# Kernel optimization log

Measured on AMD Instinct MI355X. Metric: run time of the kernel, lower is better.

## Reference

```python
import jax, jax.numpy as jnp
import numpy as np

B, CAP, H, NH = 128, 65536, 512, 8
HD = H // NH
GH = H // 4  # gate hidden


def setup_inputs() -> dict:
    key = jax.random.key(0)
    ks = jax.random.split(key, 8)
    s = 1.0 / np.sqrt(H)
    sg = 1.0 / np.sqrt(GH)
    return {
        "query": jax.random.normal(ks[0], (B, H), jnp.float32),
        "memory_keys": jax.random.normal(ks[1], (CAP, H), jnp.float32) * s,
        "memory_values": jax.random.normal(ks[2], (CAP, H), jnp.float32) * s,
        "in_proj_w": jax.random.normal(ks[3], (3 * H, H), jnp.float32) * s,
        "in_proj_b": jnp.zeros((3 * H,), jnp.float32),
        "out_proj_w": jax.random.normal(ks[4], (H, H), jnp.float32) * s,
        "out_proj_b": jnp.zeros((H,), jnp.float32),
        "gate_w1": jax.random.normal(ks[5], (GH, H), jnp.float32) * s,
        "gate_b1": jnp.zeros((GH,), jnp.float32),
        "gate_w2": jax.random.normal(ks[6], (1, GH), jnp.float32) * sg,
        "gate_b2": jnp.zeros((1,), jnp.float32),
        "usage_count": jnp.zeros((CAP,), jnp.float32),
        "last_used": jnp.zeros((CAP,), jnp.float32),
        "step_counter": 1,
    }


def reference(query, memory_keys, memory_values, in_proj_w, in_proj_b,
              out_proj_w, out_proj_b, gate_w1, gate_b1, gate_w2, gate_b2,
              usage_count, last_used, step_counter):
    # nn.MultiheadAttention packed projections: rows [0:H]=Wq, [H:2H]=Wk, [2H:3H]=Wv
    wq, wk, wv = in_proj_w[:H], in_proj_w[H:2 * H], in_proj_w[2 * H:]
    bq, bk, bv = in_proj_b[:H], in_proj_b[H:2 * H], in_proj_b[2 * H:]

    q = (query @ wq.T + bq).reshape(B, NH, HD)           # [B, h, d] (q_len = 1)
    k = (memory_keys @ wk.T + bk).reshape(CAP, NH, HD)   # [C, h, d]
    v = (memory_values @ wv.T + bv).reshape(CAP, NH, HD)  # [C, h, d]

    scores = jnp.einsum('bhd,chd->bhc', q, k) / np.sqrt(HD)  # [B, h, C]
    attn = jax.nn.softmax(scores, axis=-1)
    ctx = jnp.einsum('bhc,chd->bhd', attn, v).reshape(B, H)
    attn_out = ctx @ out_proj_w.T + out_proj_b               # [B, H]

    # usage bookkeeping: attn_weights averaged over heads, then over batch
    avg_attn = attn.mean(axis=(0, 1))                        # [C]
    new_usage = usage_count + avg_attn
    new_last = jnp.where(avg_attn > 1e-3,
                         jnp.float32(step_counter), last_used)

    # gating MLP: Linear -> ReLU -> Linear -> Sigmoid
    gate = jax.nn.sigmoid(
        jax.nn.relu(query @ gate_w1.T + gate_b1) @ gate_w2.T + gate_b2)  # [B, 1]
    memory_output = gate * attn_out                          # [B, H]
    return memory_output, new_usage, new_last
```

## Files before the change

kernel.cpp:

```cpp
#include <hip/hip_runtime.h>
#include <stdint.h>


typedef __bf16 b16x8 __attribute__((ext_vector_type(8)));
typedef float f32x4 __attribute__((ext_vector_type(4)));

static __device__ __forceinline__ unsigned short f2bf(float f) {
  return __builtin_bit_cast(unsigned short, (__bf16)f);
}

static __device__ __forceinline__ f32x4 MFMA(b16x8 a, b16x8 b, f32x4 c) {
  return __builtin_amdgcn_mfma_f32_16x16x32_bf16(a, b, c, 0, 0, 0);
}

#define GLL16(g, l)                                                          \
  __builtin_amdgcn_global_load_lds(                                          \
      (const __attribute__((address_space(1))) void*)(g),                    \
      (__attribute__((address_space(3))) void*)(l), 16, 0, 0)

#define SBAR() __builtin_amdgcn_sched_barrier(0)

__global__ void k_convert_w(const float* __restrict__ w, unsigned short* __restrict__ dst) {
  int i = blockIdx.x * 256 + threadIdx.x;
  float4 v = reinterpret_cast<const float4*>(w + 512 * 512)[i];
  ushort4 o;
  o.x = f2bf(v.x); o.y = f2bf(v.y); o.z = f2bf(v.z); o.w = f2bf(v.w);
  reinterpret_cast<ushort4*>(dst)[i] = o;
}

__global__ void k_proj_q(const float* __restrict__ query, const float* __restrict__ w,
                         const float* __restrict__ bias, unsigned short* __restrict__ qout) {
  __shared__ float qs[512];
  int b = blockIdx.x, j = threadIdx.x;
  qs[j] = query[b * 512 + j];
  __syncthreads();
  float acc = bias[j];
  const float4* q4 = reinterpret_cast<const float4*>(qs);
  const float4* w4 = reinterpret_cast<const float4*>(w + j * 512);
#pragma unroll 8
  for (int i = 0; i < 128; ++i) {
    float4 a = q4[i], c = w4[i];
    acc += a.x * c.x + a.y * c.y + a.z * c.z + a.w * c.w;
  }
  qout[b * 512 + j] = f2bf(acc);
}

__global__ void k_gate(const float* __restrict__ query, const float* __restrict__ w1,
                       const float* __restrict__ b1, const float* __restrict__ w2,
                       const float* __restrict__ b2, float* __restrict__ gate) {
  __shared__ float qs[512];
  __shared__ float red[2];
  int b = blockIdx.x, j = threadIdx.x;
  qs[j] = query[b * 512 + j];
  qs[j + 128] = query[b * 512 + j + 128];
  qs[j + 256] = query[b * 512 + j + 256];
  qs[j + 384] = query[b * 512 + j + 384];
  __syncthreads();
  float acc = b1[j];
  const float4* q4 = reinterpret_cast<const float4*>(qs);
  const float4* w4 = reinterpret_cast<const float4*>(w1 + j * 512);
#pragma unroll 8
  for (int i = 0; i < 128; ++i) {
    float4 a = q4[i], c = w4[i];
    acc += a.x * c.x + a.y * c.y + a.z * c.z + a.w * c.w;
  }
  float t = fmaxf(acc, 0.f) * w2[j];
#pragma unroll
  for (int off = 1; off < 64; off <<= 1) t += __shfl_xor(t, off, 64);
  if ((j & 63) == 0) red[j >> 6] = t;
  __syncthreads();
  if (j == 0) {
    float z = red[0] + red[1] + b2[0];
    gate[b] = 1.f / (1.f + __builtin_amdgcn_exp2f(-z * 1.44269504088896f));
  }
}

__global__ __launch_bounds__(512, 2) void k_proj_kv(
    const float* __restrict__ mk, const float* __restrict__ mv,
    const unsigned short* __restrict__ wkb, const unsigned short* __restrict__ wvb,
    const float* __restrict__ in_b,
    unsigned short* __restrict__ kout, unsigned short* __restrict__ vtout) {
  const int p = blockIdx.x;
  const int isV = p & 1;
  const int c0 = (p >> 1) * 128;
  const float* Ag = isV ? mv : mk;
  const unsigned short* W = isV ? wvb : wkb;
  const float* bias = in_b + (isV ? 1024 : 512);
  const int tid = threadIdx.x;
  const int w = tid >> 6, lane = tid & 63;
  const int wr = w >> 2, wc = w & 3;
  const int ln = tid & 15, g = (tid & 63) >> 4;

  __shared__ __align__(16) unsigned short AL[65536];
  __shared__ __align__(16) unsigned short WL[4][4096];

  const int wrow = 16 * w + (lane >> 2);
  const int wcs = (lane & 3) ^ ((wrow >> 1) & 3);
  const unsigned short* wsrc = W + (size_t)wrow * 512 + wcs * 8;
  const int wdst = w * 512;

  GLL16(wsrc, &WL[0][wdst]);
  GLL16(wsrc + 32, &WL[1][wdst]);

#pragma unroll 4
  for (int c = 0; c < 16; ++c) {
    int row = c * 8 + w;
    const float* src = Ag + (size_t)(c0 + row) * 512 + lane * 8;
    float4 f0 = *reinterpret_cast<const float4*>(src);
    float4 f1 = *reinterpret_cast<const float4*>(src + 4);
    b16x8 v;
    v[0] = (__bf16)f0.x; v[1] = (__bf16)f0.y; v[2] = (__bf16)f0.z; v[3] = (__bf16)f0.w;
    v[4] = (__bf16)f1.x; v[5] = (__bf16)f1.y; v[6] = (__bf16)f1.z; v[7] = (__bf16)f1.w;
    int chunk = lane ^ (row & 7);
    *reinterpret_cast<b16x8*>(&AL[row * 512 + chunk * 8]) = v;
  }
  __syncthreads();

#pragma unroll
  for (int jt = 0; jt < 4; ++jt) {
    const int j0 = jt * 128;
    f32x4 acc[4][2];
#pragma unroll
    for (int m = 0; m < 4; ++m)
#pragma unroll
      for (int n = 0; n < 2; ++n) acc[m][n] = {0.f, 0.f, 0.f, 0.f};

#pragma unroll
    for (int kk = 0; kk < 16; ++kk) {
      const int t = jt * 16 + kk;
      const int tn = (t + 2 <= 63) ? t + 2 : 63;
      const int slot = (t + 2) & 3;
      GLL16(wsrc + (size_t)(tn >> 4) * 65536 + (tn & 15) * 32, &WL[slot][wdst]);
      SBAR();
      asm volatile("s_waitcnt vmcnt(2)" ::: "memory");
      SBAR();
      __builtin_amdgcn_s_barrier();
      SBAR();
      b16x8 af[4], wf[2];
#pragma unroll
      for (int m = 0; m < 4; ++m) {
        int r = 64 * wr + 16 * m + ln;
        int ch = (kk * 4 + g) ^ (r & 7);
        af[m] = *reinterpret_cast<const b16x8*>(&AL[r * 512 + ch * 8]);
      }
#pragma unroll
      for (int n = 0; n < 2; ++n) {
        int r = 32 * wc + 16 * n + ln;
        wf[n] = *reinterpret_cast<const b16x8*>(&WL[t & 3][r * 32 + ((g ^ ((r >> 1) & 3)) << 3)]);
      }
      if (!isV) {
#pragma unroll
        for (int m = 0; m < 4; ++m)
#pragma unroll
          for (int n = 0; n < 2; ++n) acc[m][n] = MFMA(wf[n], af[m], acc[m][n]);
      } else {
#pragma unroll
        for (int m = 0; m < 4; ++m)
#pragma unroll
          for (int n = 0; n < 2; ++n) acc[m][n] = MFMA(af[m], wf[n], acc[m][n]);
      }
    }

    if (!isV) {
#pragma unroll
      for (int m = 0; m < 4; ++m) {
        int c = c0 + 64 * wr + 16 * m + ln;
#pragma unroll
        for (int n = 0; n < 2; ++n) {
          int jb = j0 + 32 * wc + 16 * n + 4 * g;
          float4 bb = *reinterpret_cast<const float4*>(&bias[jb]);
          ushort4 o;
          o.x = f2bf(acc[m][n][0] + bb.x);
          o.y = f2bf(acc[m][n][1] + bb.y);
          o.z = f2bf(acc[m][n][2] + bb.z);
          o.w = f2bf(acc[m][n][3] + bb.w);
          *reinterpret_cast<ushort4*>(&kout[(size_t)c * 512 + jb]) = o;
        }
      }
    } else {
#pragma unroll
      for (int n = 0; n < 2; ++n) {
        int j = j0 + 32 * wc + 16 * n + ln;
        float bj = bias[j];
#pragma unroll
        for (int m = 0; m < 4; ++m) {
          int cb = c0 + 64 * wr + 16 * m + 4 * g;
          ushort4 o;
          o.x = f2bf(acc[m][n][0] + bj);
          o.y = f2bf(acc[m][n][1] + bj);
          o.z = f2bf(acc[m][n][2] + bj);
          o.w = f2bf(acc[m][n][3] + bj);
          *reinterpret_cast<ushort4*>(&vtout[(size_t)j * 65536 + cb]) = o;
        }
      }
    }
  }
  asm volatile("s_waitcnt vmcnt(0)" ::: "memory");
}

__global__ __launch_bounds__(256) void k_attn1(
    const unsigned short* __restrict__ kb, const unsigned short* __restrict__ vt,
    const unsigned short* __restrict__ qb,
    float* __restrict__ l_ws, float* __restrict__ ctxT) {
  const int h = blockIdx.y, cg = blockIdx.x;
  const int tid = threadIdx.x;
  const int wv = tid >> 6, wr = wv >> 1, wc = wv & 1;
  const int ln = tid & 15, g = (tid & 63) >> 4;
  __shared__ __align__(16) unsigned short kS[128 * 64];
  __shared__ __align__(16) unsigned short pS[128 * 128];
  __shared__ __align__(16) unsigned short vS[64 * 128];
  const float SC = 0.125f * 1.44269504088896f;

  b16x8 qf[4][2];
#pragma unroll
  for (int n = 0; n < 4; ++n)
#pragma unroll
    for (int ks = 0; ks < 2; ++ks) {
      int b = 64 * wc + 16 * n + ln;
      qf[n][ks] = *reinterpret_cast<const b16x8*>(&qb[(size_t)b * 512 + h * 64 + ks * 32 + g * 8]);
    }
  f32x4 pacc[2][4];
#pragma unroll
  for (int m = 0; m < 2; ++m)
#pragma unroll
    for (int n = 0; n < 4; ++n) pacc[m][n] = {0.f, 0.f, 0.f, 0.f};
  float lsum[4] = {0.f, 0.f, 0.f, 0.f};

  for (int it = 0; it < 8; ++it) {
    int c0g = cg * 1024 + it * 128;
#pragma unroll
    for (int i = 0; i < 4; ++i) {
      int fl = i * 256 + tid, row = fl >> 3, p8 = fl & 7;
      uint4 d = *reinterpret_cast<const uint4*>(&kb[(size_t)(c0g + row) * 512 + h * 64 + p8 * 8]);
      *reinterpret_cast<uint4*>(&kS[(row * 8 + (p8 ^ (row & 7))) * 8]) = d;
    }
#pragma unroll
    for (int i = 0; i < 4; ++i) {
      int fl = i * 256 + tid, row = fl >> 4, p16 = fl & 15;
      uint4 d = *reinterpret_cast<const uint4*>(&vt[(size_t)(h * 64 + row) * 65536 + c0g + p16 * 8]);
      *reinterpret_cast<uint4*>(&vS[(row * 16 + (p16 ^ (row & 7))) * 8]) = d;
    }
    __syncthreads();

    f32x4 sacc[4][4];
#pragma unroll
    for (int m = 0; m < 4; ++m)
#pragma unroll
      for (int n = 0; n < 4; ++n) sacc[m][n] = {0.f, 0.f, 0.f, 0.f};
#pragma unroll
    for (int ks = 0; ks < 2; ++ks) {
      b16x8 a[4];
#pragma unroll
      for (int m = 0; m < 4; ++m) {
        int row = 64 * wr + 16 * m + ln;
        a[m] = *reinterpret_cast<const b16x8*>(&kS[(row * 8 + ((ks * 4 + g) ^ (row & 7))) * 8]);
      }
#pragma unroll
      for (int m = 0; m < 4; ++m)
#pragma unroll
        for (int n = 0; n < 4; ++n) sacc[m][n] = MFMA(a[m], qf[n][ks], sacc[m][n]);
    }
#pragma unroll
    for (int m = 0; m < 4; ++m)
#pragma unroll
      for (int n = 0; n < 4; ++n) {
        float p0 = __builtin_amdgcn_exp2f(sacc[m][n][0] * SC);
        float p1 = __builtin_amdgcn_exp2f(sacc[m][n][1] * SC);
        float p2 = __builtin_amdgcn_exp2f(sacc[m][n][2] * SC);
        float p3 = __builtin_amdgcn_exp2f(sacc[m][n][3] * SC);
        lsum[n] += (p0 + p1) + (p2 + p3);
        int b = 64 * wc + 16 * n + ln;
        int c = 64 * wr + 16 * m + 4 * g;
        int base = b * 128 + (((c >> 3) ^ (b & 7)) * 8) + (c & 7);
        ushort2 lo, hi;
        lo.x = f2bf(p0); lo.y = f2bf(p1);
        hi.x = f2bf(p2); hi.y = f2bf(p3);
        *reinterpret_cast<ushort2*>(&pS[base]) = lo;
        *reinterpret_cast<ushort2*>(&pS[base + 2]) = hi;
      }
    __syncthreads();
#pragma unroll
    for (int ks = 0; ks < 4; ++ks) {
      b16x8 av[2], bp[4];
#pragma unroll
      for (int m = 0; m < 2; ++m) {
        int row = 32 * wr + 16 * m + ln;
        av[m] = *reinterpret_cast<const b16x8*>(&vS[(row * 16 + ((ks * 4 + g) ^ (row & 7))) * 8]);
      }
#pragma unroll
      for (int n = 0; n < 4; ++n) {
        int row = 64 * wc + 16 * n + ln;
        bp[n] = *reinterpret_cast<const b16x8*>(&pS[(row * 16 + ((ks * 4 + g) ^ (row & 7))) * 8]);
      }
#pragma unroll
      for (int m = 0; m < 2; ++m)
#pragma unroll
        for (int n = 0; n < 4; ++n) pacc[m][n] = MFMA(av[m], bp[n], pacc[m][n]);
    }
    __syncthreads();
  }
#pragma unroll
  for (int n = 0; n < 4; ++n) {
    float v = lsum[n];
    v += __shfl_xor(v, 16, 64);
    v += __shfl_xor(v, 32, 64);
    if ((tid & 63) < 16) atomicAdd(&l_ws[h * 128 + 64 * wc + 16 * n + ln], v);
  }
#pragma unroll
  for (int m = 0; m < 2; ++m)
#pragma unroll
    for (int n = 0; n < 4; ++n)
#pragma unroll
      for (int r = 0; r < 4; ++r) {
        int d = 32 * wr + 16 * m + 4 * g + r;
        int b = 64 * wc + 16 * n + ln;
        atomicAdd(&ctxT[(h * 64 + d) * 128 + b], pacc[m][n][r]);
      }
}

__global__ __launch_bounds__(256) void k_attn2(
    const unsigned short* __restrict__ kb, const unsigned short* __restrict__ qb,
    const float* __restrict__ l_ws, float* __restrict__ avgA) {
  const int h = blockIdx.y, cg = blockIdx.x;
  const int tid = threadIdx.x;
  const int wv = tid >> 6, wr = wv >> 1, wc = wv & 1;
  const int ln = tid & 15, g = (tid & 63) >> 4;
  __shared__ __align__(16) unsigned short kS[128 * 64];
  __shared__ float wS[128];
  const float SC = 0.125f * 1.44269504088896f;
  if (tid < 128) wS[tid] = 1.f / l_ws[h * 128 + tid];
  b16x8 qf[4][2];
#pragma unroll
  for (int n = 0; n < 4; ++n)
#pragma unroll
    for (int ks = 0; ks < 2; ++ks) {
      int b = 64 * wc + 16 * n + ln;
      qf[n][ks] = *reinterpret_cast<const b16x8*>(&qb[(size_t)b * 512 + h * 64 + ks * 32 + g * 8]);
    }
  __syncthreads();
  float wn[4];
#pragma unroll
  for (int n = 0; n < 4; ++n) wn[n] = wS[64 * wc + 16 * n + ln];

  for (int it = 0; it < 8; ++it) {
    int c0g = cg * 1024 + it * 128;
#pragma unroll
    for (int i = 0; i < 4; ++i) {
      int fl = i * 256 + tid, row = fl >> 3, p8 = fl & 7;
      uint4 d = *reinterpret_cast<const uint4*>(&kb[(size_t)(c0g + row) * 512 + h * 64 + p8 * 8]);
      *reinterpret_cast<uint4*>(&kS[(row * 8 + (p8 ^ (row & 7))) * 8]) = d;
    }
    __syncthreads();
    f32x4 sacc[4][4];
#pragma unroll
    for (int m = 0; m < 4; ++m)
#pragma unroll
      for (int n = 0; n < 4; ++n) sacc[m][n] = {0.f, 0.f, 0.f, 0.f};
#pragma unroll
    for (int ks = 0; ks < 2; ++ks) {
      b16x8 a[4];
#pragma unroll
      for (int m = 0; m < 4; ++m) {
        int row = 64 * wr + 16 * m + ln;
        a[m] = *reinterpret_cast<const b16x8*>(&kS[(row * 8 + ((ks * 4 + g) ^ (row & 7))) * 8]);
      }
#pragma unroll
      for (int m = 0; m < 4; ++m)
#pragma unroll
        for (int n = 0; n < 4; ++n) sacc[m][n] = MFMA(a[m], qf[n][ks], sacc[m][n]);
    }
#pragma unroll
    for (int m = 0; m < 4; ++m) {
      float s0 = 0.f, s1 = 0.f, s2 = 0.f, s3 = 0.f;
#pragma unroll
      for (int n = 0; n < 4; ++n) {
        s0 += __builtin_amdgcn_exp2f(sacc[m][n][0] * SC) * wn[n];
        s1 += __builtin_amdgcn_exp2f(sacc[m][n][1] * SC) * wn[n];
        s2 += __builtin_amdgcn_exp2f(sacc[m][n][2] * SC) * wn[n];
        s3 += __builtin_amdgcn_exp2f(sacc[m][n][3] * SC) * wn[n];
      }
#pragma unroll
      for (int off = 1; off < 16; off <<= 1) {
        s0 += __shfl_xor(s0, off, 64);
        s1 += __shfl_xor(s1, off, 64);
        s2 += __shfl_xor(s2, off, 64);
        s3 += __shfl_xor(s3, off, 64);
      }
      if (ln == 0) {
        int c = c0g + 64 * wr + 16 * m + 4 * g;
        atomicAdd(&avgA[c], s0);
        atomicAdd(&avgA[c + 1], s1);
        atomicAdd(&avgA[c + 2], s2);
        atomicAdd(&avgA[c + 3], s3);
      }
    }
    __syncthreads();
  }
}

__global__ void k_finalize(const float* __restrict__ ctxT, const float* __restrict__ l_ws,
                           const float* __restrict__ wout, const float* __restrict__ bout,
                           const float* __restrict__ gate, float* __restrict__ out) {
  __shared__ float cs[512];
  int b = blockIdx.x, j = threadIdx.x;
  cs[j] = ctxT[j * 128 + b] / l_ws[(j >> 6) * 128 + b];
  __syncthreads();
  float acc = bout[j];
  const float4* c4 = reinterpret_cast<const float4*>(cs);
  const float4* w4 = reinterpret_cast<const float4*>(wout + j * 512);
#pragma unroll 8
  for (int i = 0; i < 128; ++i) {
    float4 a = c4[i], c = w4[i];
    acc += a.x * c.x + a.y * c.y + a.z * c.z + a.w * c.w;
  }
  out[b * 512 + j] = gate[b] * acc;
}

__global__ void k_usage(const float* __restrict__ avgA, const float* __restrict__ usage,
                        const float* __restrict__ last, const int* __restrict__ step,
                        float* __restrict__ out_usage, float* __restrict__ out_last) {
  int c = blockIdx.x * 256 + threadIdx.x;
  float avg = avgA[c] * (1.f / 1024.f);
  out_usage[c] = usage[c] + avg;
  out_last[c] = (avg > 0.001f) ? (float)step[0] : last[c];
}

extern "C" void kernel_launch(void* const* d_in, const int* in_sizes, int n_in,
                              void* d_out, int out_size, void* d_ws, size_t ws_size,
                              hipStream_t stream) {
  const float* query = (const float*)d_in[0];
  const float* mk    = (const float*)d_in[1];
  const float* mv    = (const float*)d_in[2];
  const float* in_w  = (const float*)d_in[3];
  const float* in_b  = (const float*)d_in[4];
  const float* out_w = (const float*)d_in[5];
  const float* out_b = (const float*)d_in[6];
  const float* gw1   = (const float*)d_in[7];
  const float* gb1   = (const float*)d_in[8];
  const float* gw2   = (const float*)d_in[9];
  const float* gb2   = (const float*)d_in[10];
  const float* usage = (const float*)d_in[11];
  const float* last  = (const float*)d_in[12];
  const int*   step  = (const int*)d_in[13];

  char* ws = (char*)d_ws;
  unsigned short* qb  = (unsigned short*)(ws);
  unsigned short* wkb = (unsigned short*)(ws + 131072);
  unsigned short* wvb = (unsigned short*)(ws + 655360);
  unsigned short* kb  = (unsigned short*)(ws + 1179648);
  unsigned short* vt  = (unsigned short*)(ws + 68288512);
  float* l_ws = (float*)(ws + 135397376);
  float* ctxT = (float*)(ws + 135401472);
  float* avgA = (float*)(ws + 135663616);
  float* gate = (float*)(ws + 135925760);
  float* out = (float*)d_out;

  hipMemsetAsync(ws + 135397376, 0, 4096 + 262144 + 262144, stream);

  k_convert_w<<<512, 256, 0, stream>>>(in_w, wkb);
  k_proj_q<<<128, 512, 0, stream>>>(query, in_w, in_b, qb);
  k_gate<<<128, 128, 0, stream>>>(query, gw1, gb1, gw2, gb2, gate);
  k_proj_kv<<<1024, 512, 0, stream>>>(mk, mv, wkb, wvb, in_b, kb, vt);
  k_attn1<<<dim3(64, 8), 256, 0, stream>>>(kb, vt, qb, l_ws, ctxT);
  k_attn2<<<dim3(64, 8), 256, 0, stream>>>(kb, qb, l_ws, avgA);
  k_finalize<<<128, 512, 0, stream>>>(ctxT, l_ws, out_w, out_b, gate, out);
  k_usage<<<256, 256, 0, stream>>>(avgA, usage, last, step, out + 65536, out + 131072);
}
```

Before: 345.7 us.

## Batch small GEMV kernels by 8 rows and give each wave private weight buffers

The q-projection, gate and finalize kernels now each handle 8 batch rows per block, so every weight row read from global memory is reused 8 times and the grid shrinks from 128 to 16 blocks. In the K/V projection kernel each wave now stages its own slice of the weight tile into a per-wave double buffer instead of a shared 4-slot ring, which removes the block-wide s_barrier on every k-step. The cost is fewer blocks (less parallelism) in the small kernels, and the per-wave buffers load weight rows redundantly across waves. The launch bound changes from 2 to 1 blocks per CU.

```diff
diff --git a/kernel.cpp b/kernel.cpp
--- a/kernel.cpp
+++ b/kernel.cpp
@@ -28,54 +28,77 @@
   reinterpret_cast<ushort4*>(dst)[i] = o;
 }
 
-__global__ void k_proj_q(const float* __restrict__ query, const float* __restrict__ w,
-                         const float* __restrict__ bias, unsigned short* __restrict__ qout) {
-  __shared__ float qs[512];
-  int b = blockIdx.x, j = threadIdx.x;
-  qs[j] = query[b * 512 + j];
+__global__ __launch_bounds__(512) void k_proj_q(const float* __restrict__ query,
+                                                const float* __restrict__ w,
+                                                const float* __restrict__ bias,
+                                                unsigned short* __restrict__ qout) {
+  __shared__ float qs[8][512];
+  const int b0 = blockIdx.x * 8, t = threadIdx.x;
+#pragma unroll
+  for (int r = 0; r < 8; ++r) qs[r][t] = query[(size_t)(b0 + r) * 512 + t];
   __syncthreads();
-  float acc = bias[j];
-  const float4* q4 = reinterpret_cast<const float4*>(qs);
-  const float4* w4 = reinterpret_cast<const float4*>(w + j * 512);
-#pragma unroll 8
+  const int j = t;
+  float bj = bias[j];
+  float acc[8];
+#pragma unroll
+  for (int r = 0; r < 8; ++r) acc[r] = bj;
+  const float4* w4 = reinterpret_cast<const float4*>(w + (size_t)j * 512);
+#pragma unroll 4
   for (int i = 0; i < 128; ++i) {
-    float4 a = q4[i], c = w4[i];
-    acc += a.x * c.x + a.y * c.y + a.z * c.z + a.w * c.w;
-  }
-  qout[b * 512 + j] = f2bf(acc);
+    float4 c = w4[i];
+#pragma unroll
+    for (int r = 0; r < 8; ++r) {
+      float4 a = reinterpret_cast<const float4*>(qs[r])[i];
+      acc[r] += a.x * c.x + a.y * c.y + a.z * c.z + a.w * c.w;
+    }
+  }
+#pragma unroll
+  for (int r = 0; r < 8; ++r) qout[(size_t)(b0 + r) * 512 + j] = f2bf(acc[r]);
 }
 
 __global__ void k_gate(const float* __restrict__ query, const float* __restrict__ w1,
                        const float* __restrict__ b1, const float* __restrict__ w2,
                        const float* __restrict__ b2, float* __restrict__ gate) {
-  __shared__ float qs[512];
-  __shared__ float red[2];
-  int b = blockIdx.x, j = threadIdx.x;
-  qs[j] = query[b * 512 + j];
-  qs[j + 128] = query[b * 512 + j + 128];
-  qs[j + 256] = query[b * 512 + j + 256];
-  qs[j + 384] = query[b * 512 + j + 384];
+  __shared__ float qs[8][512];
+  __shared__ float red[2][8];
+  const int b0 = blockIdx.x * 8, t = threadIdx.x;
+#pragma unroll
+  for (int u = 0; u < 32; ++u) {
+    int idx = u * 128 + t;
+    qs[idx >> 9][idx & 511] = query[(size_t)(b0 + (idx >> 9)) * 512 + (idx & 511)];
+  }
   __syncthreads();
-  float acc = b1[j];
-  const float4* q4 = reinterpret_cast<const float4*>(qs);
-  const float4* w4 = reinterpret_cast<const float4*>(w1 + j * 512);
-#pragma unroll 8
+  const int j = t;
+  float bj = b1[j];
+  float acc[8];
+#pragma unroll
+  for (int r = 0; r < 8; ++r) acc[r] = bj;
+  const float4* w4 = reinterpret_cast<const float4*>(w1 + (size_t)j * 512);
+#pragma unroll 4
   for (int i = 0; i < 128; ++i) {
-    float4 a = q4[i], c = w4[i];
-    acc += a.x * c.x + a.y * c.y + a.z * c.z + a.w * c.w;
-  }
-  float t = fmaxf(acc, 0.f) * w2[j];
-#pragma unroll
-  for (int off = 1; off < 64; off <<= 1) t += __shfl_xor(t, off, 64);
-  if ((j & 63) == 0) red[j >> 6] = t;
+    float4 c = w4[i];
+#pragma unroll
+    for (int r = 0; r < 8; ++r) {
+      float4 a = reinterpret_cast<const float4*>(qs[r])[i];
+      acc[r] += a.x * c.x + a.y * c.y + a.z * c.z + a.w * c.w;
+    }
+  }
+  float w2j = w2[j];
+#pragma unroll
+  for (int r = 0; r < 8; ++r) {
+    float v = fmaxf(acc[r], 0.f) * w2j;
+#pragma unroll
+    for (int off = 1; off < 64; off <<= 1) v += __shfl_xor(v, off, 64);
+    if ((t & 63) == 0) red[t >> 6][r] = v;
+  }
   __syncthreads();
-  if (j == 0) {
-    float z = red[0] + red[1] + b2[0];
-    gate[b] = 1.f / (1.f + __builtin_amdgcn_exp2f(-z * 1.44269504088896f));
-  }
-}
-
-__global__ __launch_bounds__(512, 2) void k_proj_kv(
+  if (t < 8) {
+    float z = red[0][t] + red[1][t] + b2[0];
+    gate[b0 + t] = 1.f / (1.f + __builtin_amdgcn_exp2f(-z * 1.44269504088896f));
+  }
+}
+
+__global__ __launch_bounds__(512, 1) void k_proj_kv(
     const float* __restrict__ mk, const float* __restrict__ mv,
     const unsigned short* __restrict__ wkb, const unsigned short* __restrict__ wvb,
     const float* __restrict__ in_b,
@@ -92,15 +115,14 @@
   const int ln = tid & 15, g = (tid & 63) >> 4;
 
   __shared__ __align__(16) unsigned short AL[65536];
-  __shared__ __align__(16) unsigned short WL[4][4096];
-
-  const int wrow = 16 * w + (lane >> 2);
-  const int wcs = (lane & 3) ^ ((wrow >> 1) & 3);
-  const unsigned short* wsrc = W + (size_t)wrow * 512 + wcs * 8;
-  const int wdst = w * 512;
-
-  GLL16(wsrc, &WL[0][wdst]);
-  GLL16(wsrc + 32, &WL[1][wdst]);
+  __shared__ __align__(16) unsigned short WLp[8][2][1024];
+
+  const int srw0 = 32 * wc + ln;
+  const int srw1 = srw0 + 16;
+  const int colo = g * 8;
+
+  GLL16(W + (size_t)srw0 * 512 + colo, &WLp[w][0][0]);
+  GLL16(W + (size_t)srw1 * 512 + colo, &WLp[w][0][512]);
 
 #pragma unroll 4
   for (int c = 0; c < 16; ++c) {
@@ -118,7 +140,6 @@
 
 #pragma unroll
   for (int jt = 0; jt < 4; ++jt) {
-    const int j0 = jt * 128;
     f32x4 acc[4][2];
 #pragma unroll
     for (int m = 0; m < 4; ++m)
@@ -128,13 +149,13 @@
 #pragma unroll
     for (int kk = 0; kk < 16; ++kk) {
       const int t = jt * 16 + kk;
-      const int tn = (t + 2 <= 63) ? t + 2 : 63;
-      const int slot = (t + 2) & 3;
-      GLL16(wsrc + (size_t)(tn >> 4) * 65536 + (tn & 15) * 32, &WL[slot][wdst]);
+      const int tn = (t < 63) ? t + 1 : 63;
+      const int sl = (t + 1) & 1;
+      const int jn = tn >> 4, kn = tn & 15;
+      GLL16(W + (size_t)(jn * 128 + srw0) * 512 + kn * 32 + colo, &WLp[w][sl][0]);
+      GLL16(W + (size_t)(jn * 128 + srw1) * 512 + kn * 32 + colo, &WLp[w][sl][512]);
       SBAR();
       asm volatile("s_waitcnt vmcnt(2)" ::: "memory");
-      SBAR();
-      __builtin_amdgcn_s_barrier();
       SBAR();
       b16x8 af[4], wf[2];
 #pragma unroll
@@ -144,10 +165,8 @@
         af[m] = *reinterpret_cast<const b16x8*>(&AL[r * 512 + ch * 8]);
       }
 #pragma unroll
-      for (int n = 0; n < 2; ++n) {
-        int r = 32 * wc + 16 * n + ln;
-        wf[n] = *reinterpret_cast<const b16x8*>(&WL[t & 3][r * 32 + ((g ^ ((r >> 1) & 3)) << 3)]);
-      }
+      for (int n = 0; n < 2; ++n)
+        wf[n] = *reinterpret_cast<const b16x8*>(&WLp[w][t & 1][n * 512 + lane * 8]);
       if (!isV) {
 #pragma unroll
         for (int m = 0; m < 4; ++m)
@@ -161,6 +180,7 @@
       }
     }
 
+    const int j0 = jt * 128;
     if (!isV) {
 #pragma unroll
       for (int m = 0; m < 4; ++m) {
@@ -398,22 +418,35 @@
   }
 }
 
-__global__ void k_finalize(const float* __restrict__ ctxT, const float* __restrict__ l_ws,
-                           const float* __restrict__ wout, const float* __restrict__ bout,
-                           const float* __restrict__ gate, float* __restrict__ out) {
-  __shared__ float cs[512];
-  int b = blockIdx.x, j = threadIdx.x;
-  cs[j] = ctxT[j * 128 + b] / l_ws[(j >> 6) * 128 + b];
+__global__ __launch_bounds__(512) void k_finalize(
+    const float* __restrict__ ctxT, const float* __restrict__ l_ws,
+    const float* __restrict__ wout, const float* __restrict__ bout,
+    const float* __restrict__ gate, float* __restrict__ out) {
+  __shared__ float cs[8][512];
+  const int b0 = blockIdx.x * 8, t = threadIdx.x;
+#pragma unroll
+  for (int r = 0; r < 8; ++r) {
+    int b = b0 + r;
+    cs[r][t] = ctxT[t * 128 + b] / l_ws[(t >> 6) * 128 + b];
+  }
   __syncthreads();
-  float acc = bout[j];
-  const float4* c4 = reinterpret_cast<const float4*>(cs);
-  const float4* w4 = reinterpret_cast<const float4*>(wout + j * 512);
-#pragma unroll 8
+  const int j = t;
+  float bj = bout[j];
+  float acc[8];
+#pragma unroll
+  for (int r = 0; r < 8; ++r) acc[r] = bj;
+  const float4* w4 = reinterpret_cast<const float4*>(wout + (size_t)j * 512);
+#pragma unroll 4
   for (int i = 0; i < 128; ++i) {
-    float4 a = c4[i], c = w4[i];
-    acc += a.x * c.x + a.y * c.y + a.z * c.z + a.w * c.w;
-  }
-  out[b * 512 + j] = gate[b] * acc;
+    float4 c = w4[i];
+#pragma unroll
+    for (int r = 0; r < 8; ++r) {
+      float4 a = reinterpret_cast<const float4*>(cs[r])[i];
+      acc[r] += a.x * c.x + a.y * c.y + a.z * c.z + a.w * c.w;
+    }
+  }
+#pragma unroll
+  for (int r = 0; r < 8; ++r) out[(size_t)(b0 + r) * 512 + j] = gate[b0 + r] * acc[r];
 }
 
 __global__ void k_usage(const float* __restrict__ avgA, const float* __restrict__ usage,
@@ -458,11 +491,11 @@
   hipMemsetAsync(ws + 135397376, 0, 4096 + 262144 + 262144, stream);
 
   k_convert_w<<<512, 256, 0, stream>>>(in_w, wkb);
-  k_proj_q<<<128, 512, 0, stream>>>(query, in_w, in_b, qb);
-  k_gate<<<128, 128, 0, stream>>>(query, gw1, gb1, gw2, gb2, gate);
+  k_proj_q<<<16, 512, 0, stream>>>(query, in_w, in_b, qb);
+  k_gate<<<16, 128, 0, stream>>>(query, gw1, gb1, gw2, gb2, gate);
   k_proj_kv<<<1024, 512, 0, stream>>>(mk, mv, wkb, wvb, in_b, kb, vt);
   k_attn1<<<dim3(64, 8), 256, 0, stream>>>(kb, vt, qb, l_ws, ctxT);
   k_attn2<<<dim3(64, 8), 256, 0, stream>>>(kb, qb, l_ws, avgA);
-  k_finalize<<<128, 512, 0, stream>>>(ctxT, l_ws, out_w, out_b, gate, out);
+  k_finalize<<<16, 512, 0, stream>>>(ctxT, l_ws, out_w, out_b, gate, out);
   k_usage<<<256, 256, 0, stream>>>(avgA, usage, last, step, out + 65536, out + 131072);
 }
```

After: 414.3 us. 19.8% more time.

## Halve K/V projection tile to 64 rows with 256-thread blocks and double-buffered weights

Applied to the files above, without the earlier changes.

Changes the K/V projection kernel from 128-row tiles with 512 threads to 64-row tiles with 256 threads, doubling the grid. The weight staging drops from a 4-slot prefetch ring to a 2-slot double buffer loading one step ahead, with an extra barrier after each MFMA step to protect the slot being reused. Shared memory per block roughly halves, which should let more blocks sit on each CU and improve latency hiding. In exchange, each weight tile is reused across fewer activation rows, so weight traffic from L2 doubles, and the extra per-step barrier adds synchronisation.

```diff
diff --git a/kernel.cpp b/kernel.cpp
--- a/kernel.cpp
+++ b/kernel.cpp
@@ -75,36 +75,35 @@
   }
 }
 
-__global__ __launch_bounds__(512, 2) void k_proj_kv(
+__global__ __launch_bounds__(256, 2) void k_proj_kv(
     const float* __restrict__ mk, const float* __restrict__ mv,
     const unsigned short* __restrict__ wkb, const unsigned short* __restrict__ wvb,
     const float* __restrict__ in_b,
     unsigned short* __restrict__ kout, unsigned short* __restrict__ vtout) {
   const int p = blockIdx.x;
   const int isV = p & 1;
-  const int c0 = (p >> 1) * 128;
+  const int c0 = (p >> 1) * 64;
   const float* Ag = isV ? mv : mk;
   const unsigned short* W = isV ? wvb : wkb;
   const float* bias = in_b + (isV ? 1024 : 512);
   const int tid = threadIdx.x;
   const int w = tid >> 6, lane = tid & 63;
-  const int wr = w >> 2, wc = w & 3;
   const int ln = tid & 15, g = (tid & 63) >> 4;
 
-  __shared__ __align__(16) unsigned short AL[65536];
-  __shared__ __align__(16) unsigned short WL[4][4096];
-
-  const int wrow = 16 * w + (lane >> 2);
-  const int wcs = (lane & 3) ^ ((wrow >> 1) & 3);
-  const unsigned short* wsrc = W + (size_t)wrow * 512 + wcs * 8;
-  const int wdst = w * 512;
-
-  GLL16(wsrc, &WL[0][wdst]);
-  GLL16(wsrc + 32, &WL[1][wdst]);
+  __shared__ __align__(16) unsigned short AL[32768];
+  __shared__ __align__(16) unsigned short WL[2][4096];
+
+  const int srow = 16 * w + (lane >> 2);
+  const int csrc = (lane & 3) ^ ((srow >> 1) & 3);
+  const int wd0 = w * 512;
+  const int wd1 = 2048 + w * 512;
+
+  GLL16(W + (size_t)srow * 512 + csrc * 8, &WL[0][wd0]);
+  GLL16(W + (size_t)(64 + srow) * 512 + csrc * 8, &WL[0][wd1]);
 
 #pragma unroll 4
   for (int c = 0; c < 16; ++c) {
-    int row = c * 8 + w;
+    int row = c * 4 + w;
     const float* src = Ag + (size_t)(c0 + row) * 512 + lane * 8;
     float4 f0 = *reinterpret_cast<const float4*>(src);
     float4 f1 = *reinterpret_cast<const float4*>(src + 4);
@@ -118,7 +117,6 @@
 
 #pragma unroll
   for (int jt = 0; jt < 4; ++jt) {
-    const int j0 = jt * 128;
     f32x4 acc[4][2];
 #pragma unroll
     for (int m = 0; m < 4; ++m)
@@ -128,9 +126,10 @@
 #pragma unroll
     for (int kk = 0; kk < 16; ++kk) {
       const int t = jt * 16 + kk;
-      const int tn = (t + 2 <= 63) ? t + 2 : 63;
-      const int slot = (t + 2) & 3;
-      GLL16(wsrc + (size_t)(tn >> 4) * 65536 + (tn & 15) * 32, &WL[slot][wdst]);
+      const int tn = (t < 63) ? t + 1 : 63;
+      const int jn = tn >> 4, kn = tn & 15, sl = tn & 1;
+      GLL16(W + (size_t)(jn * 128 + srow) * 512 + kn * 32 + csrc * 8, &WL[sl][wd0]);
+      GLL16(W + (size_t)(jn * 128 + 64 + srow) * 512 + kn * 32 + csrc * 8, &WL[sl][wd1]);
       SBAR();
       asm volatile("s_waitcnt vmcnt(2)" ::: "memory");
       SBAR();
@@ -139,14 +138,15 @@
       b16x8 af[4], wf[2];
 #pragma unroll
       for (int m = 0; m < 4; ++m) {
-        int r = 64 * wr + 16 * m + ln;
+        int r = 16 * m + ln;
         int ch = (kk * 4 + g) ^ (r & 7);
         af[m] = *reinterpret_cast<const b16x8*>(&AL[r * 512 + ch * 8]);
       }
 #pragma unroll
       for (int n = 0; n < 2; ++n) {
-        int r = 32 * wc + 16 * n + ln;
-        wf[n] = *reinterpret_cast<const b16x8*>(&WL[t & 3][r * 32 + ((g ^ ((r >> 1) & 3)) << 3)]);
+        int r = 32 * w + 16 * n + ln;
+        int ch = g ^ ((r >> 1) & 3);
+        wf[n] = *reinterpret_cast<const b16x8*>(&WL[t & 1][r * 32 + ch * 8]);
       }
       if (!isV) {
 #pragma unroll
@@ -159,15 +159,19 @@
 #pragma unroll
           for (int n = 0; n < 2; ++n) acc[m][n] = MFMA(af[m], wf[n], acc[m][n]);
       }
-    }
-
+      SBAR();
+      __builtin_amdgcn_s_barrier();
+      SBAR();
+    }
+
+    const int j0 = jt * 128;
     if (!isV) {
 #pragma unroll
       for (int m = 0; m < 4; ++m) {
-        int c = c0 + 64 * wr + 16 * m + ln;
+        int c = c0 + 16 * m + ln;
 #pragma unroll
         for (int n = 0; n < 2; ++n) {
-          int jb = j0 + 32 * wc + 16 * n + 4 * g;
+          int jb = j0 + 32 * w + 16 * n + 4 * g;
           float4 bb = *reinterpret_cast<const float4*>(&bias[jb]);
           ushort4 o;
           o.x = f2bf(acc[m][n][0] + bb.x);
@@ -180,11 +184,11 @@
     } else {
 #pragma unroll
       for (int n = 0; n < 2; ++n) {
-        int j = j0 + 32 * wc + 16 * n + ln;
+        int j = j0 + 32 * w + 16 * n + ln;
         float bj = bias[j];
 #pragma unroll
         for (int m = 0; m < 4; ++m) {
-          int cb = c0 + 64 * wr + 16 * m + 4 * g;
+          int cb = c0 + 16 * m + 4 * g;
           ushort4 o;
           o.x = f2bf(acc[m][n][0] + bj);
           o.y = f2bf(acc[m][n][1] + bj);
@@ -460,7 +464,7 @@
   k_convert_w<<<512, 256, 0, stream>>>(in_w, wkb);
   k_proj_q<<<128, 512, 0, stream>>>(query, in_w, in_b, qb);
   k_gate<<<128, 128, 0, stream>>>(query, gw1, gb1, gw2, gb2, gate);
-  k_proj_kv<<<1024, 512, 0, stream>>>(mk, mv, wkb, wvb, in_b, kb, vt);
+  k_proj_kv<<<2048, 256, 0, stream>>>(mk, mv, wkb, wvb, in_b, kb, vt);
   k_attn1<<<dim3(64, 8), 256, 0, stream>>>(kb, vt, qb, l_ws, ctxT);
   k_attn2<<<dim3(64, 8), 256, 0, stream>>>(kb, qb, l_ws, avgA);
   k_finalize<<<128, 512, 0, stream>>>(ctxT, l_ws, out_w, out_b, gate, out);
```

After: 344.6 us (median of 2 runs). No clear change (-0.3%).
